# Optimization experiments

Hardware: AMD Instinct MI355X
Metric: run time of the kernel (lower is better)

The kernel has to match this reference:

```python
import jax, jax.numpy as jnp
import numpy as np

DECAY = 0.99
EPS = 1e-05
BETA = 0.25
N_CODES = 1024
CODE_DIM = 128


def setup_inputs() -> dict:
    key = jax.random.key(0)
    k1, k2, k3, k4 = jax.random.split(key, 4)
    z_e = jax.random.normal(k1, (32, CODE_DIM, 32, 32), dtype=jnp.float32)
    embed = jax.random.normal(k2, (N_CODES, CODE_DIM), dtype=jnp.float32)
    cluster_size = jax.random.uniform(k3, (N_CODES,), dtype=jnp.float32) * 10.0
    embed_avg = jax.random.normal(k4, (N_CODES, CODE_DIM), dtype=jnp.float32)
    return {"z_e": z_e, "embed": embed, "cluster_size": cluster_size, "embed_avg": embed_avg}


def reference(z_e, embed, cluster_size, embed_avg):
    B, C, H, W = z_e.shape
    n_codes = embed.shape[0]
    # (B,C,H,W) -> (B*H*W, C)
    flat = jnp.transpose(z_e, (0, 2, 3, 1)).reshape(-1, C).astype(jnp.float32)
    e = embed.astype(jnp.float32)
    d = (flat ** 2).sum(1, keepdims=True) - 2.0 * flat @ e.T + (e ** 2).sum(1)
    idx = jnp.argmin(d, axis=1)
    z_q = embed[idx].reshape(B, H, W, C)
    z_q = jnp.transpose(z_q, (0, 3, 1, 2))  # (B,C,H,W)

    # ---- EMA codebook update (training branch, no-grad in torch) ----
    counts = jax.ops.segment_sum(jnp.ones_like(idx, dtype=jnp.float32), idx,
                                 num_segments=n_codes)
    new_cluster_size = cluster_size * DECAY + (1.0 - DECAY) * counts
    embed_sum = jax.ops.segment_sum(flat, idx, num_segments=n_codes)  # == (flat.T @ one_hot).T
    new_embed_avg = embed_avg * DECAY + (1.0 - DECAY) * embed_sum
    n = new_cluster_size.sum()
    denom = n + n_codes * EPS
    cs = (new_cluster_size + EPS) / denom * n
    cs_safe = jnp.maximum(cs, EPS)[:, None]
    embed_normalized = new_embed_avg / cs_safe
    embed_normalized = jnp.nan_to_num(embed_normalized, nan=0.0, posinf=1.0, neginf=-1.0)
    new_embed = jnp.clip(embed_normalized, -2.0, 2.0)

    # straight-through estimator
    z_q_st = z_e + jax.lax.stop_gradient(z_q - z_e)
    diff = jax.lax.stop_gradient(z_q_st).astype(jnp.float32) - z_e.astype(jnp.float32)
    loss = BETA * jnp.mean(diff ** 2)

    return (z_q_st, loss, idx.reshape(B, H, W), z_q, z_e,
            new_embed, new_cluster_size, new_embed_avg)
```

## Files before the change

kernel.cpp:

```cpp
#include <hip/hip_runtime.h>

#define DECAY 0.99f
#define ONE_MINUS_DECAY 0.01f
#define EPSF 1e-5f
#define BETA 0.25f

constexpr int M_ = 32768;
constexpr int N_ = 1024;
constexpr int K_ = 128;

typedef _Float16 f16;
typedef f16 f16x8 __attribute__((ext_vector_type(8)));
typedef float f32x4 __attribute__((ext_vector_type(4)));

#define GLOAD_LDS(g, l) __builtin_amdgcn_global_load_lds( \
    (const __attribute__((address_space(1))) void*)(g),   \
    (__attribute__((address_space(3))) void*)(l), 16, 0, 0)

#define PINS(p) { unsigned _t2 = m1 > (p) ? m1 : (p); m1 = m1 < (p) ? m1 : (p); \
                  unsigned _t3 = m2 > _t2 ? m2 : _t2;  m2 = m2 < _t2 ? m2 : _t2; \
                  m3 = m3 < _t3 ? m3 : _t3; }

constexpr size_t WS_FLAT   = 0;
constexpr size_t WS_XH     = WS_FLAT   + (size_t)M_ * K_ * 4;
constexpr size_t WS_XL     = WS_XH     + (size_t)M_ * K_ * 2;
constexpr size_t WS_EH     = WS_XL     + (size_t)M_ * K_ * 2;
constexpr size_t WS_NL     = WS_EH     + (size_t)N_ * K_ * 2;
constexpr size_t WS_PPK    = WS_NL     + (size_t)N_ * 4;
constexpr size_t WS_IDX    = WS_PPK    + (size_t)4 * M_ * 16;
constexpr size_t WS_COUNTS = WS_IDX    + (size_t)M_ * 4;
constexpr size_t WS_CUR    = WS_COUNTS + (size_t)N_ * 4;
constexpr size_t WS_ESUM   = WS_CUR    + (size_t)N_ * 4;
constexpr size_t WS_OFFS   = WS_ESUM   + (size_t)N_ * K_ * 4;
constexpr size_t WS_ROWS   = WS_OFFS   + (size_t)N_ * 4;
constexpr size_t WS_LPART  = WS_ROWS   + (size_t)M_ * 4;
constexpr size_t WS_NSUM   = WS_LPART  + (size_t)4096 * 8;

constexpr size_t O_ZQST = 0;
constexpr size_t O_LOSS = O_ZQST + (size_t)M_ * K_;
constexpr size_t O_IDX  = O_LOSS + 1;
constexpr size_t O_ZQ   = O_IDX  + (size_t)M_;
constexpr size_t O_ZE   = O_ZQ   + (size_t)M_ * K_;
constexpr size_t O_EMB  = O_ZE   + (size_t)M_ * K_;
constexpr size_t O_NCS  = O_EMB  + (size_t)N_ * K_;
constexpr size_t O_NEA  = O_NCS  + (size_t)N_;

__global__ void ecvt_kernel(const float* __restrict__ embed,
                            f16* __restrict__ eh, float* __restrict__ nl,
                            uint4* __restrict__ zero8k) {
    int j = blockIdx.x, lane = threadIdx.x;
    int gid = j * 64 + lane;
    if (gid < 512) zero8k[gid] = make_uint4(0u, 0u, 0u, 0u);
    const float* e = embed + (size_t)j * K_;
    float a = e[lane], b = e[lane + 64];
    float s = a * a + b * b;
    #pragma unroll
    for (int off = 32; off; off >>= 1) s += __shfl_down(s, off);
    if (lane == 0) nl[j] = s;
    eh[(size_t)j * K_ + lane]      = (f16)(-2.f * a);
    eh[(size_t)j * K_ + lane + 64] = (f16)(-2.f * b);
}

__global__ void transpose_kernel(const float* __restrict__ ze,
                                 float* __restrict__ flat,
                                 f16* __restrict__ xh, f16* __restrict__ xl,
                                 float* __restrict__ out_ze) {
    __shared__ float tile[128][33];
    int b = blockIdx.x >> 5, h = blockIdx.x & 31;
    const size_t base = (size_t)b * 131072 + (size_t)h * 32;
    int t = threadIdx.x;
    #pragma unroll
    for (int i = 0; i < 4; ++i) {
        int q = i * 256 + t;
        int c = q >> 3, w4 = (q & 7) * 4;
        float4 v = *(const float4*)(ze + base + (size_t)c * 1024 + w4);
        tile[c][w4 + 0] = v.x; tile[c][w4 + 1] = v.y;
        tile[c][w4 + 2] = v.z; tile[c][w4 + 3] = v.w;
        *(float4*)(out_ze + base + (size_t)c * 1024 + w4) = v;
    }
    __syncthreads();
    const int r0 = b * 1024 + h * 32;
    #pragma unroll
    for (int i = 0; i < 2; ++i) {
        int w = (t >> 4) + i * 16;
        int c0 = (t & 15) * 8;
        int r = r0 + w;
        float vv[8];
        #pragma unroll
        for (int j = 0; j < 8; ++j) vv[j] = tile[c0 + j][w];
        *(float4*)(flat + (size_t)r * K_ + c0)     = make_float4(vv[0], vv[1], vv[2], vv[3]);
        *(float4*)(flat + (size_t)r * K_ + c0 + 4) = make_float4(vv[4], vv[5], vv[6], vv[7]);
        f16x8 hv, lv;
        #pragma unroll
        for (int j = 0; j < 8; ++j) {
            f16 hh = (f16)vv[j];
            hv[j] = hh;
            lv[j] = (f16)(vv[j] - (float)hh);
        }
        size_t xa = (size_t)r * K_ + ((((c0 >> 3) ^ (r & 15)) << 3));
        *(f16x8*)(xh + xa) = hv;
        *(f16x8*)(xl + xa) = lv;
    }
}

__global__ __launch_bounds__(256, 3)
void nn_kernel(const f16* __restrict__ xh_g, const f16* __restrict__ xl_g,
               const f16* __restrict__ eh, const float* __restrict__ nl,
               uint4* __restrict__ p_pk) {
    __shared__ __align__(16) f16 xbh[64 * 128];
    __shared__ __align__(16) f16 xbl[64 * 128];
    __shared__ uint4 pm[4][64];
    const int t = threadIdx.x;
    const int wave = t >> 6, lane = t & 63;
    const int crow = lane & 15, g = lane >> 4;
    const int c0 = blockIdx.y * 256 + wave * 64;

    f16x8 efh[4][4];
    #pragma unroll
    for (int m = 0; m < 4; ++m)
        #pragma unroll
        for (int kt = 0; kt < 4; ++kt)
            efh[m][kt] = *(const f16x8*)(eh + (size_t)(c0 + m * 16 + crow) * K_ + kt * 32 + g * 8);
    f32x4 nlpre[4];
    #pragma unroll
    for (int m = 0; m < 4; ++m) {
        f32x4 v = *(const f32x4*)(nl + c0 + m * 16 + g * 4);
        nlpre[m] = v * 1024.f + 1048576.f;
    }
    const unsigned cbase = (unsigned)(c0 + g * 4);

    auto stage = [&](int bt) {
        const size_t tb = (size_t)(blockIdx.x * 4 + bt) * 8192;
        #pragma unroll
        for (int i = 0; i < 4; ++i) {
            int q = wave * 4 + i;
            GLOAD_LDS(xh_g + tb + q * 512 + lane * 8, &xbh[q * 512]);
            GLOAD_LDS(xl_g + tb + q * 512 + lane * 8, &xbl[q * 512]);
        }
    };

    stage(0);
    __syncthreads();
    for (int bt = 0; bt < 4; ++bt) {
        const int R0 = (blockIdx.x * 4 + bt) * 64;
        #pragma unroll
        for (int st = 0; st < 4; ++st) {
            f32x4 acc[4];
            #pragma unroll
            for (int m = 0; m < 4; ++m) acc[m] = (f32x4){0.f, 0.f, 0.f, 0.f};
            #pragma unroll
            for (int kt = 0; kt < 4; ++kt) {
                int off = (st * 16 + crow) * 128 + ((((kt << 2) + g) ^ crow) << 3);
                f16x8 bh = *(const f16x8*)&xbh[off];
                f16x8 bl = *(const f16x8*)&xbl[off];
                #pragma unroll
                for (int m = 0; m < 4; ++m) {
                    acc[m] = __builtin_amdgcn_mfma_f32_16x16x32_f16(efh[m][kt], bh, acc[m], 0, 0, 0);
                    acc[m] = __builtin_amdgcn_mfma_f32_16x16x32_f16(efh[m][kt], bl, acc[m], 0, 0, 0);
                }
            }
            unsigned m1 = ~0u, m2 = ~0u, m3 = ~0u;
            #pragma unroll
            for (int m = 0; m < 4; ++m)
                #pragma unroll
                for (int q = 0; q < 4; ++q) {
                    float fq = fmaf(acc[m][q], 1024.f, nlpre[m][q]);
                    unsigned p = (((unsigned)fq) << 10) + cbase + (unsigned)(m * 16 + q);
                    PINS(p);
                }
            #pragma unroll
            for (int d = 16; d <= 32; d <<= 1) {
                unsigned o1 = (unsigned)__shfl_xor((int)m1, d);
                unsigned o2 = (unsigned)__shfl_xor((int)m2, d);
                unsigned o3 = (unsigned)__shfl_xor((int)m3, d);
                PINS(o1); PINS(o2); PINS(o3);
            }
            if (lane < 16) pm[wave][st * 16 + crow] = make_uint4(m1, m2, m3, 0u);
        }
        __syncthreads();
        if (bt < 3) stage(bt + 1);
        if (lane < 16) {
            int row = wave * 16 + lane;
            uint4 a = pm[0][row];
            unsigned m1 = a.x, m2 = a.y, m3 = a.z;
            #pragma unroll
            for (int w = 1; w < 4; ++w) {
                uint4 b = pm[w][row];
                PINS(b.x); PINS(b.y); PINS(b.z);
            }
            p_pk[(size_t)blockIdx.y * M_ + R0 + row] = make_uint4(m1, m2, m3, 0u);
        }
        __syncthreads();
    }
}

__global__ void reduce_refine_kernel(const uint4* __restrict__ p_pk,
                                     const float* __restrict__ flat,
                                     const float* __restrict__ embed,
                                     const float* __restrict__ nl,
                                     int* __restrict__ idxws, float* __restrict__ out_idx,
                                     int* __restrict__ counts) {
    int r = blockIdx.x * 256 + threadIdx.x;
    uint4 a = p_pk[r];
    unsigned m1 = a.x, m2 = a.y, m3 = a.z;
    #pragma unroll
    for (int y = 1; y < 4; ++y) {
        uint4 b = p_pk[(size_t)y * M_ + r];
        PINS(b.x); PINS(b.y); PINS(b.z);
    }
    int i1 = (int)(m1 & 1023u);
    if ((m2 >> 10) - (m1 >> 10) <= 512u) {
        int i2 = (int)(m2 & 1023u), i3 = (int)(m3 & 1023u);
        const float* x  = flat  + (size_t)r * K_;
        const float* e1 = embed + (size_t)i1 * K_;
        const float* e2 = embed + (size_t)i2 * K_;
        const float* e3 = embed + (size_t)i3 * K_;
        float d1 = 0.f, d2 = 0.f, d3 = 0.f;
        for (int k = 0; k < K_; ++k) {
            float xv = x[k];
            d1 = fmaf(xv, e1[k], d1);
            d2 = fmaf(xv, e2[k], d2);
            d3 = fmaf(xv, e3[k], d3);
        }
        float s1 = fmaf(-2.f, d1, nl[i1]);
        float s2 = fmaf(-2.f, d2, nl[i2]);
        float s3 = fmaf(-2.f, d3, nl[i3]);
        float bs = s1; int bi = i1;
        if (s2 < bs || (s2 == bs && i2 < bi)) { bs = s2; bi = i2; }
        if (s3 < bs || (s3 == bs && i3 < bi)) { bs = s3; bi = i3; }
        i1 = bi;
    }
    idxws[r] = i1;
    out_idx[r] = (float)i1;
    atomicAdd(counts + i1, 1);
}

__global__ void gather_kernel(const float* __restrict__ ze,
                              const float* __restrict__ embed,
                              const int* __restrict__ idxws,
                              float* __restrict__ out_st, float* __restrict__ out_zq,
                              double* __restrict__ lpart) {
    int q = blockIdx.x * 256 + threadIdx.x;
    int o0 = q * 4;
    float4 zev = *(const float4*)(ze + o0);
    const float zv[4] = {zev.x, zev.y, zev.z, zev.w};
    float st4[4], zq4[4];
    double ls = 0.0;
    #pragma unroll
    for (int e = 0; e < 4; ++e) {
        int o = o0 + e;
        int r = (o >> 17) * 1024 + (o & 1023);
        int c = (o >> 10) & 127;
        int j = idxws[r];
        float zq = embed[(size_t)j * K_ + c];
        float st = zv[e] + (zq - zv[e]);
        st4[e] = st; zq4[e] = zq;
        float diff = st - zv[e];
        ls += (double)diff * (double)diff;
    }
    *(float4*)(out_st + o0) = make_float4(st4[0], st4[1], st4[2], st4[3]);
    *(float4*)(out_zq + o0) = make_float4(zq4[0], zq4[1], zq4[2], zq4[3]);
    __shared__ double red[256];
    red[threadIdx.x] = ls;
    __syncthreads();
    for (int s = 128; s; s >>= 1) {
        if (threadIdx.x < s) red[threadIdx.x] += red[threadIdx.x + s];
        __syncthreads();
    }
    if (threadIdx.x == 0) lpart[blockIdx.x] = red[0];
}

__global__ void ema_a_kernel(const float* __restrict__ cluster_size,
                             const int* __restrict__ counts,
                             float* __restrict__ out_ncs, float* __restrict__ nws,
                             const double* __restrict__ lpart, float* __restrict__ out_loss,
                             int* __restrict__ offs) {
    int j = threadIdx.x;
    int cnt = counts[j];
    float ncs = cluster_size[j] * DECAY + ONE_MINUS_DECAY * (float)cnt;
    out_ncs[j] = ncs;
    __shared__ float red[1024];
    __shared__ double dred[1024];
    __shared__ int sc[1024];
    red[j] = ncs;
    sc[j] = cnt;
    double s = 0.0;
    #pragma unroll
    for (int i = 0; i < 4; ++i) s += lpart[j * 4 + i];
    dred[j] = s;
    __syncthreads();
    for (int d = 1; d < 1024; d <<= 1) {
        int v = (j >= d) ? sc[j - d] : 0;
        __syncthreads();
        sc[j] += v;
        __syncthreads();
    }
    offs[j] = sc[j] - cnt;
    for (int st = 512; st; st >>= 1) {
        if (j < st) { red[j] += red[j + st]; dred[j] += dred[j + st]; }
        __syncthreads();
    }
    if (j == 0) {
        nws[0] = red[0];
        out_loss[0] = (float)((double)BETA * (dred[0] / 4194304.0));
    }
}

__global__ void bucket_kernel(const int* __restrict__ idxws, const int* __restrict__ offs,
                              int* __restrict__ cur, int* __restrict__ rows,
                              float4* __restrict__ esum_z) {
    __shared__ int lcnt[N_];
    __shared__ int lbase[N_];
    int t = threadIdx.x;
    esum_z[blockIdx.x * 256 + t] = make_float4(0.f, 0.f, 0.f, 0.f);
    #pragma unroll
    for (int i = 0; i < 4; ++i) lcnt[i * 256 + t] = 0;
    __syncthreads();
    int r = blockIdx.x * 256 + t;
    int j = idxws[r];
    atomicAdd(&lcnt[j], 1);
    __syncthreads();
    #pragma unroll
    for (int i = 0; i < 4; ++i) {
        int c = i * 256 + t;
        int n = lcnt[c];
        lbase[c] = n ? atomicAdd(cur + c, n) : 0;
        lcnt[c] = 0;
    }
    __syncthreads();
    int p = atomicAdd(&lcnt[j], 1) + lbase[j];
    rows[offs[j] + p] = r;
}

__global__ void chunksum_kernel(const float* __restrict__ flat,
                                const int* __restrict__ rows,
                                const int* __restrict__ idxws,
                                float* __restrict__ esum) {
    __shared__ int srid[64];
    __shared__ int scd[65];
    int k = threadIdx.x;
    int b = blockIdx.x;
    if (k < 64) {
        int r = rows[b * 64 + k];
        srid[k] = r;
        scd[k] = idxws[r];
    }
    if (k == 64) scd[64] = -1;
    __syncthreads();
    float acc = 0.f;
    #pragma unroll 1
    for (int i0 = 0; i0 < 64; i0 += 8) {
        float v[8];
        #pragma unroll
        for (int i = 0; i < 8; ++i)
            v[i] = flat[(size_t)srid[i0 + i] * K_ + k];
        #pragma unroll
        for (int i = 0; i < 8; ++i) {
            acc += v[i];
            int p = i0 + i;
            if (scd[p + 1] != scd[p]) {
                atomicAdd(esum + (size_t)scd[p] * K_ + k, acc);
                acc = 0.f;
            }
        }
    }
}

__global__ void ema_b_kernel(const float* __restrict__ embed_avg,
                             const float* __restrict__ esum,
                             const float* __restrict__ out_ncs,
                             const float* __restrict__ nws,
                             float* __restrict__ out_nea, float* __restrict__ out_emb) {
    int o = blockIdx.x * 256 + threadIdx.x;
    int j = o >> 7;
    float navg = embed_avg[o] * DECAY + ONE_MINUS_DECAY * esum[o];
    out_nea[o] = navg;
    float n = nws[0];
    float denom = n + 1024.0f * EPSF;
    float cs = (out_ncs[j] + EPSF) / denom * n;
    float cs_safe = fmaxf(cs, EPSF);
    float v = navg / cs_safe;
    if (v != v) v = 0.f;
    v = fminf(fmaxf(v, -2.f), 2.f);
    out_emb[o] = v;
}

extern "C" void kernel_launch(void* const* d_in, const int* in_sizes, int n_in,
                              void* d_out, int out_size, void* d_ws, size_t ws_size,
                              hipStream_t stream) {
    const float* z_e          = (const float*)d_in[0];
    const float* embed        = (const float*)d_in[1];
    const float* cluster_size = (const float*)d_in[2];
    const float* embed_avg    = (const float*)d_in[3];
    float* out = (float*)d_out;
    char*  ws  = (char*)d_ws;

    float*  flat   = (float*)(ws + WS_FLAT);
    f16*    xhp    = (f16*)  (ws + WS_XH);
    f16*    xlp    = (f16*)  (ws + WS_XL);
    f16*    ehp    = (f16*)  (ws + WS_EH);
    float*  nlp    = (float*)(ws + WS_NL);
    uint4*  p_pk   = (uint4*)(ws + WS_PPK);
    int*    idxws  = (int*)  (ws + WS_IDX);
    int*    counts = (int*)  (ws + WS_COUNTS);
    int*    cur    = (int*)  (ws + WS_CUR);
    float*  esum   = (float*)(ws + WS_ESUM);
    int*    offs   = (int*)  (ws + WS_OFFS);
    int*    rows   = (int*)  (ws + WS_ROWS);
    double* lpart  = (double*)(ws + WS_LPART);
    float*  nws    = (float*)(ws + WS_NSUM);

    ecvt_kernel<<<N_, 64, 0, stream>>>(embed, ehp, nlp, (uint4*)(ws + WS_COUNTS));
    transpose_kernel<<<1024, 256, 0, stream>>>(z_e, flat, xhp, xlp, out + O_ZE);
    nn_kernel<<<dim3(128, 4), 256, 0, stream>>>(xhp, xlp, ehp, nlp, p_pk);
    reduce_refine_kernel<<<M_ / 256, 256, 0, stream>>>(p_pk, flat, embed, nlp,
                                                       idxws, out + O_IDX, counts);
    gather_kernel<<<4096, 256, 0, stream>>>(z_e, embed, idxws,
                                            out + O_ZQST, out + O_ZQ, lpart);
    ema_a_kernel<<<1, 1024, 0, stream>>>(cluster_size, counts, out + O_NCS, nws,
                                         lpart, out + O_LOSS, offs);
    bucket_kernel<<<M_ / 256, 256, 0, stream>>>(idxws, offs, cur, rows,
                                                (float4*)(ws + WS_ESUM));
    chunksum_kernel<<<M_ / 64, K_, 0, stream>>>(flat, rows, idxws, esum);
    ema_b_kernel<<<(N_ * K_) / 256, 256, 0, stream>>>(embed_avg, esum, out + O_NCS, nws,
                                                      out + O_NEA, out + O_EMB);
}
```

Measured before the change: 104.2 us.

## Drop low-half fp16 split in NN search, fuse embed conversion into transpose

Removes the hi/lo fp16 split of the inputs, so the distance MFMA pass uses only the high fp16 half. This halves the MFMA count, the LDS staging and the workspace traffic, and the launch bound rises from 3 to 4 blocks per CU. The codebook conversion and norm computation now run inside the transpose kernel, which saves one launch. The gather kernel loads the four indices with a single int4 read. Candidate accuracy falls, so correctness now relies on the later refine step catching near-ties.

```diff
diff --git a/kernel.cpp b/kernel.cpp
--- a/kernel.cpp
+++ b/kernel.cpp
@@ -23,8 +23,7 @@
 
 constexpr size_t WS_FLAT   = 0;
 constexpr size_t WS_XH     = WS_FLAT   + (size_t)M_ * K_ * 4;
-constexpr size_t WS_XL     = WS_XH     + (size_t)M_ * K_ * 2;
-constexpr size_t WS_EH     = WS_XL     + (size_t)M_ * K_ * 2;
+constexpr size_t WS_EH     = WS_XH     + (size_t)M_ * K_ * 2;
 constexpr size_t WS_NL     = WS_EH     + (size_t)N_ * K_ * 2;
 constexpr size_t WS_PPK    = WS_NL     + (size_t)N_ * 4;
 constexpr size_t WS_IDX    = WS_PPK    + (size_t)4 * M_ * 16;
@@ -45,30 +44,29 @@
 constexpr size_t O_NCS  = O_EMB  + (size_t)N_ * K_;
 constexpr size_t O_NEA  = O_NCS  + (size_t)N_;
 
-__global__ void ecvt_kernel(const float* __restrict__ embed,
-                            f16* __restrict__ eh, float* __restrict__ nl,
-                            uint4* __restrict__ zero8k) {
-    int j = blockIdx.x, lane = threadIdx.x;
-    int gid = j * 64 + lane;
-    if (gid < 512) zero8k[gid] = make_uint4(0u, 0u, 0u, 0u);
-    const float* e = embed + (size_t)j * K_;
-    float a = e[lane], b = e[lane + 64];
-    float s = a * a + b * b;
-    #pragma unroll
-    for (int off = 32; off; off >>= 1) s += __shfl_down(s, off);
-    if (lane == 0) nl[j] = s;
-    eh[(size_t)j * K_ + lane]      = (f16)(-2.f * a);
-    eh[(size_t)j * K_ + lane + 64] = (f16)(-2.f * b);
-}
-
 __global__ void transpose_kernel(const float* __restrict__ ze,
+                                 const float* __restrict__ embed,
                                  float* __restrict__ flat,
-                                 f16* __restrict__ xh, f16* __restrict__ xl,
-                                 float* __restrict__ out_ze) {
+                                 f16* __restrict__ xh,
+                                 float* __restrict__ out_ze,
+                                 f16* __restrict__ eh, float* __restrict__ nl,
+                                 uint4* __restrict__ zero8k) {
     __shared__ float tile[128][33];
-    int b = blockIdx.x >> 5, h = blockIdx.x & 31;
+    __shared__ float ered[2];
+    const int j = blockIdx.x;
+    const int t = threadIdx.x;
+    if (t < 128) {
+        float a = embed[(size_t)j * K_ + t];
+        eh[(size_t)j * K_ + t] = (f16)(-2.f * a);
+        float s = a * a;
+        #pragma unroll
+        for (int off = 32; off; off >>= 1) s += __shfl_down(s, off);
+        if ((t & 63) == 0) ered[t >> 6] = s;
+    }
+    if (j < 2) zero8k[j * 256 + t] = make_uint4(0u, 0u, 0u, 0u);
+
+    int b = j >> 5, h = j & 31;
     const size_t base = (size_t)b * 131072 + (size_t)h * 32;
-    int t = threadIdx.x;
     #pragma unroll
     for (int i = 0; i < 4; ++i) {
         int q = i * 256 + t;
@@ -79,6 +77,7 @@
         *(float4*)(out_ze + base + (size_t)c * 1024 + w4) = v;
     }
     __syncthreads();
+    if (t == 0) nl[j] = ered[0] + ered[1];
     const int r0 = b * 1024 + h * 32;
     #pragma unroll
     for (int i = 0; i < 2; ++i) {
@@ -87,28 +86,22 @@
         int r = r0 + w;
         float vv[8];
         #pragma unroll
-        for (int j = 0; j < 8; ++j) vv[j] = tile[c0 + j][w];
+        for (int q = 0; q < 8; ++q) vv[q] = tile[c0 + q][w];
         *(float4*)(flat + (size_t)r * K_ + c0)     = make_float4(vv[0], vv[1], vv[2], vv[3]);
         *(float4*)(flat + (size_t)r * K_ + c0 + 4) = make_float4(vv[4], vv[5], vv[6], vv[7]);
-        f16x8 hv, lv;
-        #pragma unroll
-        for (int j = 0; j < 8; ++j) {
-            f16 hh = (f16)vv[j];
-            hv[j] = hh;
-            lv[j] = (f16)(vv[j] - (float)hh);
-        }
+        f16x8 hv;
+        #pragma unroll
+        for (int q = 0; q < 8; ++q) hv[q] = (f16)vv[q];
         size_t xa = (size_t)r * K_ + ((((c0 >> 3) ^ (r & 15)) << 3));
         *(f16x8*)(xh + xa) = hv;
-        *(f16x8*)(xl + xa) = lv;
-    }
-}
-
-__global__ __launch_bounds__(256, 3)
-void nn_kernel(const f16* __restrict__ xh_g, const f16* __restrict__ xl_g,
+    }
+}
+
+__global__ __launch_bounds__(256, 4)
+void nn_kernel(const f16* __restrict__ xh_g,
                const f16* __restrict__ eh, const float* __restrict__ nl,
                uint4* __restrict__ p_pk) {
     __shared__ __align__(16) f16 xbh[64 * 128];
-    __shared__ __align__(16) f16 xbl[64 * 128];
     __shared__ uint4 pm[4][64];
     const int t = threadIdx.x;
     const int wave = t >> 6, lane = t & 63;
@@ -135,7 +128,6 @@
         for (int i = 0; i < 4; ++i) {
             int q = wave * 4 + i;
             GLOAD_LDS(xh_g + tb + q * 512 + lane * 8, &xbh[q * 512]);
-            GLOAD_LDS(xl_g + tb + q * 512 + lane * 8, &xbl[q * 512]);
         }
     };
 
@@ -152,12 +144,9 @@
             for (int kt = 0; kt < 4; ++kt) {
                 int off = (st * 16 + crow) * 128 + ((((kt << 2) + g) ^ crow) << 3);
                 f16x8 bh = *(const f16x8*)&xbh[off];
-                f16x8 bl = *(const f16x8*)&xbl[off];
                 #pragma unroll
-                for (int m = 0; m < 4; ++m) {
+                for (int m = 0; m < 4; ++m)
                     acc[m] = __builtin_amdgcn_mfma_f32_16x16x32_f16(efh[m][kt], bh, acc[m], 0, 0, 0);
-                    acc[m] = __builtin_amdgcn_mfma_f32_16x16x32_f16(efh[m][kt], bl, acc[m], 0, 0, 0);
-                }
             }
             unsigned m1 = ~0u, m2 = ~0u, m3 = ~0u;
             #pragma unroll
@@ -244,15 +233,15 @@
     int o0 = q * 4;
     float4 zev = *(const float4*)(ze + o0);
     const float zv[4] = {zev.x, zev.y, zev.z, zev.w};
+    int rbase = (o0 >> 17) * 1024 + (o0 & 1023);
+    int c = (o0 >> 10) & 127;
+    int4 jj = *(const int4*)(idxws + rbase);
+    const int jv[4] = {jj.x, jj.y, jj.z, jj.w};
     float st4[4], zq4[4];
     double ls = 0.0;
     #pragma unroll
     for (int e = 0; e < 4; ++e) {
-        int o = o0 + e;
-        int r = (o >> 17) * 1024 + (o & 1023);
-        int c = (o >> 10) & 127;
-        int j = idxws[r];
-        float zq = embed[(size_t)j * K_ + c];
+        float zq = embed[(size_t)jv[e] * K_ + c];
         float st = zv[e] + (zq - zv[e]);
         st4[e] = st; zq4[e] = zq;
         float diff = st - zv[e];
@@ -397,7 +386,6 @@
 
     float*  flat   = (float*)(ws + WS_FLAT);
     f16*    xhp    = (f16*)  (ws + WS_XH);
-    f16*    xlp    = (f16*)  (ws + WS_XL);
     f16*    ehp    = (f16*)  (ws + WS_EH);
     float*  nlp    = (float*)(ws + WS_NL);
     uint4*  p_pk   = (uint4*)(ws + WS_PPK);
@@ -410,9 +398,9 @@
     double* lpart  = (double*)(ws + WS_LPART);
     float*  nws    = (float*)(ws + WS_NSUM);
 
-    ecvt_kernel<<<N_, 64, 0, stream>>>(embed, ehp, nlp, (uint4*)(ws + WS_COUNTS));
-    transpose_kernel<<<1024, 256, 0, stream>>>(z_e, flat, xhp, xlp, out + O_ZE);
-    nn_kernel<<<dim3(128, 4), 256, 0, stream>>>(xhp, xlp, ehp, nlp, p_pk);
+    transpose_kernel<<<1024, 256, 0, stream>>>(z_e, embed, flat, xhp, out + O_ZE,
+                                               ehp, nlp, (uint4*)(ws + WS_COUNTS));
+    nn_kernel<<<dim3(128, 4), 256, 0, stream>>>(xhp, ehp, nlp, p_pk);
     reduce_refine_kernel<<<M_ / 256, 256, 0, stream>>>(p_pk, flat, embed, nlp,
                                                        idxws, out + O_IDX, counts);
     gather_kernel<<<4096, 256, 0, stream>>>(z_e, embed, idxws,
```

Result: faster. 94.22 us (-9.6%).
